# Optimization experiments

Measured on AMD Instinct MI355X. Metric: run time of the kernel, lower is better.

The kernel has to match this reference:

```python
import jax, jax.numpy as jnp
import numpy as np

H = 40
W = 40
IN_POINTS = 36


def grid_sample_bilinear_border(img, grid):
    """PyTorch F.grid_sample(mode='bilinear', padding_mode='border', align_corners=False).
    img: (B, C, H, W); grid: (B, P, 2) with (x, y) in [-1, 1]. Returns (B, C, P)."""
    B, C, h, w = img.shape
    # unnormalize (align_corners=False): pix = ((g + 1) * size - 1) / 2
    x = ((grid[..., 0] + 1.0) * w - 1.0) * 0.5
    y = ((grid[..., 1] + 1.0) * h - 1.0) * 0.5
    # border padding: clamp coords into valid range
    x = jnp.clip(x, 0.0, w - 1.0)
    y = jnp.clip(y, 0.0, h - 1.0)
    x0f = jnp.floor(x)
    y0f = jnp.floor(y)
    wx = (x - x0f)[..., None]  # (B, P, 1)
    wy = (y - y0f)[..., None]
    x0 = x0f.astype(jnp.int32)
    y0 = y0f.astype(jnp.int32)
    x1 = jnp.minimum(x0 + 1, w - 1)
    y1 = jnp.minimum(y0 + 1, h - 1)
    imgt = img.transpose(0, 2, 3, 1)  # (B, H, W, C) for channel-last gathers
    b = jnp.arange(B)[:, None]        # (B, 1) broadcasts against (B, P)
    v00 = imgt[b, y0, x0]  # (B, P, C)
    v01 = imgt[b, y0, x1]
    v10 = imgt[b, y1, x0]
    v11 = imgt[b, y1, x1]
    out = (v00 * (1 - wx) * (1 - wy) + v01 * wx * (1 - wy)
           + v10 * (1 - wx) * wy + v11 * wx * wy)
    return out.transpose(0, 2, 1)  # (B, C, P)


def setup_inputs() -> dict:
    key = jax.random.key(0)
    ks = jax.random.split(key, 6)
    bs, c = 128, 256
    content_query = jax.random.normal(ks[0], (bs, c), dtype=jnp.float32)
    reference_point = jax.random.uniform(ks[1], (bs, 2), dtype=jnp.float32)
    feature_map = jax.random.normal(ks[2], (bs, c, H * W), dtype=jnp.float32)
    pos = jax.random.normal(ks[3], (bs, c, H * W), dtype=jnp.float32)
    # small offset weights so sampled points stay mostly in [0,1] (module inits these near zero)
    W_off = jax.random.normal(ks[4], (IN_POINTS * 2, c), dtype=jnp.float32) * 0.02
    b_off = jax.random.uniform(ks[5], (IN_POINTS * 2,), dtype=jnp.float32) - 0.5
    return {"content_query": content_query, "reference_point": reference_point,
            "feature_map": feature_map, "pos": pos, "W_off": W_off, "b_off": b_off}


def reference(content_query, reference_point, feature_map, pos, W_off, b_off):
    bs, c = content_query.shape
    # offset generator: nn.Linear(hidden_dim, in_points*2)
    xy_offsets = (content_query @ W_off.T + b_off).reshape(bs, IN_POINTS, 2)
    sampled_points = xy_offsets + reference_point[:, None, :]  # (bs, P, 2)
    fmap = feature_map.reshape(bs, c, H, W)
    pmap = pos.reshape(bs, c, H, W)
    grid = 2.0 * sampled_points - 1.0
    sampled_features = grid_sample_bilinear_border(fmap, grid)  # (bs, C, P)
    pe = grid_sample_bilinear_border(pmap, grid)                # (bs, C, P)
    return (sampled_features, pe)
```

## Files before the change

kernel.cpp:

```cpp
#include <hip/hip_runtime.h>

#define HH 40
#define WW 40
#define NP 36
#define NC 256
#define NB 128

__global__ void points_kernel(const float* __restrict__ cq,
                              const float* __restrict__ refp,
                              const float* __restrict__ Woff,
                              const float* __restrict__ boff,
                              float2* __restrict__ pts) {
    int b = blockIdx.x;
    __shared__ float q[NC];
    __shared__ float offs[2 * NP];
    for (int i = threadIdx.x; i < NC; i += blockDim.x) q[i] = cq[b * NC + i];
    __syncthreads();
    int j = threadIdx.x;
    if (j < 2 * NP) {
        const float* w = Woff + j * NC;
        float acc = 0.f;
#pragma unroll 8
        for (int k = 0; k < NC; ++k) acc = fmaf(q[k], w[k], acc);
        offs[j] = acc + boff[j];
    }
    __syncthreads();
    int p = threadIdx.x;
    if (p < NP) {
        float sx = offs[2 * p + 0] + refp[b * 2 + 0];
        float sy = offs[2 * p + 1] + refp[b * 2 + 1];
        float x = fminf(fmaxf(sx * (float)WW - 0.5f, 0.f), (float)(WW - 1));
        float y = fminf(fmaxf(sy * (float)HH - 0.5f, 0.f), (float)(HH - 1));
        pts[b * NP + p] = make_float2(x, y);
    }
}

__global__ void sample_kernel(const float* __restrict__ fmap,
                              const float* __restrict__ pmap,
                              const float2* __restrict__ pts,
                              float* __restrict__ out) {
    long tid = (long)blockIdx.x * blockDim.x + threadIdx.x;
    const long total = (long)NB * NC * NP;
    if (tid >= total) return;
    int p = (int)(tid % NP);
    long t2 = tid / NP;
    int c = (int)(t2 % NC);
    int b = (int)(t2 / NC);

    float2 xy = pts[b * NP + p];
    float x0f = floorf(xy.x), y0f = floorf(xy.y);
    float wx = xy.x - x0f, wy = xy.y - y0f;
    int x0 = (int)x0f, y0 = (int)y0f;
    int x1 = min(x0 + 1, WW - 1), y1 = min(y0 + 1, HH - 1);

    long base = ((long)b * NC + c) * (HH * WW);
    int i00 = y0 * WW + x0;
    int i01 = y0 * WW + x1;
    int i10 = y1 * WW + x0;
    int i11 = y1 * WW + x1;

    float w00 = (1.f - wx) * (1.f - wy);
    float w01 = wx * (1.f - wy);
    float w10 = (1.f - wx) * wy;
    float w11 = wx * wy;

    float f = fmap[base + i00] * w00 + fmap[base + i01] * w01 +
              fmap[base + i10] * w10 + fmap[base + i11] * w11;
    float g = pmap[base + i00] * w00 + pmap[base + i01] * w01 +
              pmap[base + i10] * w10 + pmap[base + i11] * w11;

    long oidx = ((long)b * NC + c) * NP + p;
    out[oidx] = f;
    out[(long)NB * NC * NP + oidx] = g;
}

extern "C" void kernel_launch(void* const* d_in, const int* in_sizes, int n_in,
                              void* d_out, int out_size, void* d_ws, size_t ws_size,
                              hipStream_t stream) {
    const float* cq   = (const float*)d_in[0];
    const float* refp = (const float*)d_in[1];
    const float* fmap = (const float*)d_in[2];
    const float* pmap = (const float*)d_in[3];
    const float* Woff = (const float*)d_in[4];
    const float* boff = (const float*)d_in[5];
    float* out = (float*)d_out;
    float2* pts = (float2*)d_ws;

    points_kernel<<<NB, 128, 0, stream>>>(cq, refp, Woff, boff, pts);

    const long total = (long)NB * NC * NP;
    int block = 256;
    int grid = (int)((total + block - 1) / block);
    sample_kernel<<<grid, block, 0, stream>>>(fmap, pmap, pts, out);
}
```

Measured before the change: 53.38 us.

## Precompute bilinear weights/indices per point and process four channels per thread

The points kernel now computes the four bilinear weights and flat corner indices once per (batch, point) and stores them as float4/int4 records. The sample kernel reads these records and each thread handles four channels of one point, reusing the weights and indices across them. The GEMV in the points kernel uses float4 loads. This cuts redundant per-thread index math and division work, and reduces the thread count fourfold, at the cost of less parallelism and strided output stores per thread.

```diff
diff --git a/kernel.cpp b/kernel.cpp
--- a/kernel.cpp
+++ b/kernel.cpp
@@ -6,22 +6,28 @@
 #define NC 256
 #define NB 128
 
-__global__ void points_kernel(const float* __restrict__ cq,
-                              const float* __restrict__ refp,
-                              const float* __restrict__ Woff,
-                              const float* __restrict__ boff,
-                              float2* __restrict__ pts) {
+__global__ __launch_bounds__(128) void points_kernel(
+    const float* __restrict__ cq, const float* __restrict__ refp,
+    const float* __restrict__ Woff, const float* __restrict__ boff,
+    float4* __restrict__ rec_w, int4* __restrict__ rec_i) {
     int b = blockIdx.x;
-    __shared__ float q[NC];
+    __shared__ float4 q[NC / 4];
     __shared__ float offs[2 * NP];
-    for (int i = threadIdx.x; i < NC; i += blockDim.x) q[i] = cq[b * NC + i];
+    if (threadIdx.x < NC / 4)
+        q[threadIdx.x] = ((const float4*)(cq + b * NC))[threadIdx.x];
     __syncthreads();
     int j = threadIdx.x;
     if (j < 2 * NP) {
-        const float* w = Woff + j * NC;
+        const float4* w = (const float4*)(Woff + j * NC);
         float acc = 0.f;
-#pragma unroll 8
-        for (int k = 0; k < NC; ++k) acc = fmaf(q[k], w[k], acc);
+#pragma unroll
+        for (int k = 0; k < NC / 4; ++k) {
+            float4 a = q[k], bb = w[k];
+            acc = fmaf(a.x, bb.x, acc);
+            acc = fmaf(a.y, bb.y, acc);
+            acc = fmaf(a.z, bb.z, acc);
+            acc = fmaf(a.w, bb.w, acc);
+        }
         offs[j] = acc + boff[j];
     }
     __syncthreads();
@@ -31,47 +37,43 @@
         float sy = offs[2 * p + 1] + refp[b * 2 + 1];
         float x = fminf(fmaxf(sx * (float)WW - 0.5f, 0.f), (float)(WW - 1));
         float y = fminf(fmaxf(sy * (float)HH - 0.5f, 0.f), (float)(HH - 1));
-        pts[b * NP + p] = make_float2(x, y);
+        float x0f = floorf(x), y0f = floorf(y);
+        int x0 = (int)x0f, y0 = (int)y0f;
+        int x1 = min(x0 + 1, WW - 1), y1 = min(y0 + 1, HH - 1);
+        float wx = x - x0f, wy = y - y0f;
+        rec_w[b * NP + p] = make_float4((1.f - wx) * (1.f - wy), wx * (1.f - wy),
+                                        (1.f - wx) * wy, wx * wy);
+        rec_i[b * NP + p] = make_int4(y0 * WW + x0, y0 * WW + x1,
+                                      y1 * WW + x0, y1 * WW + x1);
     }
 }
 
-__global__ void sample_kernel(const float* __restrict__ fmap,
-                              const float* __restrict__ pmap,
-                              const float2* __restrict__ pts,
-                              float* __restrict__ out) {
-    long tid = (long)blockIdx.x * blockDim.x + threadIdx.x;
-    const long total = (long)NB * NC * NP;
-    if (tid >= total) return;
-    int p = (int)(tid % NP);
-    long t2 = tid / NP;
-    int c = (int)(t2 % NC);
-    int b = (int)(t2 / NC);
+__global__ __launch_bounds__(256) void sample_kernel(
+    const float* __restrict__ fmap, const float* __restrict__ pmap,
+    const float4* __restrict__ rec_w, const int4* __restrict__ rec_i,
+    float* __restrict__ out) {
+    int tid = blockIdx.x * 256 + threadIdx.x;
+    int p = tid % NP;
+    int t2 = tid / NP;
+    int cq = t2 & 63;
+    int b = t2 >> 6;
 
-    float2 xy = pts[b * NP + p];
-    float x0f = floorf(xy.x), y0f = floorf(xy.y);
-    float wx = xy.x - x0f, wy = xy.y - y0f;
-    int x0 = (int)x0f, y0 = (int)y0f;
-    int x1 = min(x0 + 1, WW - 1), y1 = min(y0 + 1, HH - 1);
+    float4 w = rec_w[b * NP + p];
+    int4 io = rec_i[b * NP + p];
 
-    long base = ((long)b * NC + c) * (HH * WW);
-    int i00 = y0 * WW + x0;
-    int i01 = y0 * WW + x1;
-    int i10 = y1 * WW + x0;
-    int i11 = y1 * WW + x1;
+    long base = ((long)(b * NC) + cq * 4) * (HH * WW);
+    float* o1 = out + ((long)(b * NC) + cq * 4) * NP + p;
+    float* o2 = o1 + (long)NB * NC * NP;
 
-    float w00 = (1.f - wx) * (1.f - wy);
-    float w01 = wx * (1.f - wy);
-    float w10 = (1.f - wx) * wy;
-    float w11 = wx * wy;
-
-    float f = fmap[base + i00] * w00 + fmap[base + i01] * w01 +
-              fmap[base + i10] * w10 + fmap[base + i11] * w11;
-    float g = pmap[base + i00] * w00 + pmap[base + i01] * w01 +
-              pmap[base + i10] * w10 + pmap[base + i11] * w11;
-
-    long oidx = ((long)b * NC + c) * NP + p;
-    out[oidx] = f;
-    out[(long)NB * NC * NP + oidx] = g;
+#pragma unroll
+    for (int k = 0; k < 4; ++k) {
+        const float* f = fmap + base + k * (HH * WW);
+        const float* g = pmap + base + k * (HH * WW);
+        float vf = f[io.x] * w.x + f[io.y] * w.y + f[io.z] * w.z + f[io.w] * w.w;
+        float vg = g[io.x] * w.x + g[io.y] * w.y + g[io.z] * w.z + g[io.w] * w.w;
+        o1[k * NP] = vf;
+        o2[k * NP] = vg;
+    }
 }
 
 extern "C" void kernel_launch(void* const* d_in, const int* in_sizes, int n_in,
@@ -84,12 +86,12 @@
     const float* Woff = (const float*)d_in[4];
     const float* boff = (const float*)d_in[5];
     float* out = (float*)d_out;
-    float2* pts = (float2*)d_ws;
 
-    points_kernel<<<NB, 128, 0, stream>>>(cq, refp, Woff, boff, pts);
+    float4* rec_w = (float4*)d_ws;
+    int4*   rec_i = (int4*)((char*)d_ws + NB * NP * 16);
 
-    const long total = (long)NB * NC * NP;
-    int block = 256;
-    int grid = (int)((total + block - 1) / block);
-    sample_kernel<<<grid, block, 0, stream>>>(fmap, pmap, pts, out);
+    points_kernel<<<NB, 128, 0, stream>>>(cq, refp, Woff, boff, rec_w, rec_i);
+
+    const int total = NB * 64 * NP;
+    sample_kernel<<<total / 256, 256, 0, stream>>>(fmap, pmap, rec_w, rec_i, out);
 }
```

Result: slower. 62.68 us (+17.4%).
